# Kernel optimization log

Measured on AMD Instinct MI355X. Metric: run time of the kernel, lower is better.

The kernel has to match this reference:

```python
import jax, jax.numpy as jnp
import numpy as np

B, N, IN_DIM, HEADS, PER_HEAD = 8, 512, 256, 4, 32
OUT_DIM = HEADS * PER_HEAD  # 128
NEG_SLOPE = 0.2


def setup_inputs() -> dict:
    key = jax.random.key(0)
    ks = jax.random.split(key, 8)
    x = jax.random.normal(ks[0], (B, N, IN_DIM), jnp.float32)
    adj = jax.random.randint(ks[1], (B, N, N), 0, 2, jnp.int32)
    sl = 1.0 / np.sqrt(IN_DIM)
    W_l = jax.random.normal(ks[2], (IN_DIM, OUT_DIM), jnp.float32) * sl  # source proj
    b_l = jnp.zeros((OUT_DIM,), jnp.float32)
    W_r = jax.random.normal(ks[3], (IN_DIM, OUT_DIM), jnp.float32) * sl  # target proj
    b_r = jnp.zeros((OUT_DIM,), jnp.float32)
    att = jax.random.normal(ks[4], (HEADS, PER_HEAD), jnp.float32) * (1.0 / np.sqrt(PER_HEAD))
    bias = jnp.zeros((OUT_DIM,), jnp.float32)
    return {"x": x, "adj": adj, "W_l": W_l, "b_l": b_l, "W_r": W_r, "b_r": b_r,
            "att": att, "bias": bias}


def _gatv2_single(x_b, adj_b, W_l, b_l, W_r, b_r, att, bias):
    # PyG GATv2Conv: remove_self_loops + add_self_loops -> diagonal forced to 1
    n = x_b.shape[0]
    adj_sl = jnp.fill_diagonal(adj_b, 1, inplace=False)
    # edge_index = adj.nonzero().t(): source = row, target = col
    m = (adj_sl != 0).T  # m[i, j]: source j feeds target i
    xl = (x_b @ W_l + b_l).reshape(n, HEADS, PER_HEAD)  # source-side features
    xr = (x_b @ W_r + b_r).reshape(n, HEADS, PER_HEAD)  # target-side features
    s = xr[:, None] + xl[None, :]                       # [i, j, H, C]
    s = jnp.where(s > 0, s, NEG_SLOPE * s)              # LeakyReLU(0.2)
    e = jnp.einsum('ijhc,hc->ijh', s, att)              # attention logits
    e = jnp.where(m[..., None], e, -jnp.inf)
    alpha = jax.nn.softmax(e, axis=1)                   # softmax over sources j
    out = jnp.einsum('ijh,jhc->ihc', alpha, xl).reshape(n, HEADS * PER_HEAD)
    return out + bias


def reference(x, adj, W_l, b_l, W_r, b_r, att, bias):
    # Sequential per-batch processing, faithful to the original Python loop
    # and keeping the [N,N,H,C] intermediate to one graph at a time.
    def one(args):
        x_b, adj_b = args
        return _gatv2_single(x_b, adj_b, W_l, b_l, W_r, b_r, att, bias)
    return jax.lax.map(one, (x, adj))  # [B, N, OUT_DIM]
```

## Files before the change

### kernel.cpp

```cpp
#include <hip/hip_runtime.h>
#include <hip/hip_bf16.h>

#define B_   8
#define N_   512
#define IND  256
#define H_   4
#define PH   32
#define OD   128
#define TI   4
#define TJ   64
#define XLS_STRIDE 132

__global__ __launch_bounds__(256, 2) void proj_kernel(
    const float* __restrict__ x,
    const float* __restrict__ Wl, const float* __restrict__ bl,
    const float* __restrict__ Wr, const float* __restrict__ br,
    const float* __restrict__ att,
    float* __restrict__ xl, float* __restrict__ xr,
    float* __restrict__ dl, float* __restrict__ dr)
{
    __shared__ float xs[8 * IND];
    const int t = threadIdx.x;
    const int row0 = blockIdx.x * 8;

    const float4* xp4 = (const float4*)(x + (size_t)row0 * IND);
    float4* xs4 = (float4*)xs;
    #pragma unroll
    for (int k = 0; k < 2; ++k)
        xs4[t + k * 256] = xp4[t + k * 256];
    __syncthreads();

    const int which = t >> 7;
    const int rg = (t >> 6) & 1;
    const int og = t & 63;
    const int o0 = og * 2;
    const int r0 = rg * 4;
    const float* W  = which ? Wr : Wl;
    const float* bb = which ? br : bl;

    float acc0[4], acc1[4];
    #pragma unroll
    for (int r = 0; r < 4; ++r) { acc0[r] = 0.f; acc1[r] = 0.f; }

    for (int k = 0; k < IND; k += 4) {
        float wf0[4], wf1[4];
        #pragma unroll
        for (int kk = 0; kk < 4; ++kk) {
            float2 wv = *(const float2*)(W + (size_t)(k + kk) * OD + o0);
            wf0[kk] = wv.x;
            wf1[kk] = wv.y;
        }
        float xv[4][4];
        #pragma unroll
        for (int r = 0; r < 4; ++r)
            *(float4*)(xv[r]) = *(const float4*)(&xs[(r0 + r) * IND + k]);
        #pragma unroll
        for (int kk = 0; kk < 4; ++kk)
            #pragma unroll
            for (int r = 0; r < 4; ++r) {
                acc0[r] = fmaf(xv[r][kk], wf0[kk], acc0[r]);
                acc1[r] = fmaf(xv[r][kk], wf1[kk], acc1[r]);
            }
    }

    const float bv0 = bb[o0];
    const float bv1 = bb[o0 + 1];
    const float a0 = att[o0];
    const float a1 = att[o0 + 1];
    float* dst = which ? xr : xl;
    float* dp  = which ? dr : dl;
    float dcon[4];
    #pragma unroll
    for (int r = 0; r < 4; ++r) {
        float y0 = acc0[r] + bv0;
        float y1 = acc1[r] + bv1;
        *(float2*)(&dst[(size_t)(row0 + r0 + r) * OD + o0]) = make_float2(y0, y1);
        dcon[r] = fmaf(a0, y0, a1 * y1);
    }
    #pragma unroll
    for (int m = 1; m < 16; m <<= 1) {
        #pragma unroll
        for (int r = 0; r < 4; ++r)
            dcon[r] += __shfl_xor(dcon[r], m);
    }
    if ((og & 15) == 0) {
        const int h = og >> 4;
        #pragma unroll
        for (int r = 0; r < 4; ++r)
            dp[(size_t)(row0 + r0 + r) * H_ + h] = dcon[r];
    }
}

__global__ __launch_bounds__(256, 2) void attn_kernel(
    const int* __restrict__ adj, const float* __restrict__ att,
    const float* __restrict__ bias,
    const float* __restrict__ xl, const float* __restrict__ xr,
    const float* __restrict__ dl, const float* __restrict__ dr,
    float* __restrict__ out)
{
    __shared__ float xls[TJ * XLS_STRIDE];
    __shared__ float masks[TJ * TI];

    const int t = threadIdx.x;
    const int b  = blockIdx.x >> 7;
    const int i0 = (blockIdx.x & 127) * TI;
    const int ch = t & 1;
    const int q  = (t >> 1) & 7;
    const int il = (t >> 4) & 3;
    const int h  = t >> 6;
    const int ig = i0 + il;
    const int cbase = h * PH + ch * 16;

    float attv[16], xrv[16];
    {
        const float* xrp = xr + ((size_t)(b * N_ + ig)) * OD + cbase;
        #pragma unroll
        for (int k = 0; k < 16; k += 4) {
            float4 v = *(const float4*)(xrp + k);
            xrv[k] = v.x; xrv[k+1] = v.y; xrv[k+2] = v.z; xrv[k+3] = v.w;
        }
        const float* ap = att + cbase;
        #pragma unroll
        for (int k = 0; k < 16; ++k) attv[k] = ap[k];
    }
    const float c0 = 0.6f * dr[((size_t)(b * N_ + ig)) * H_ + h];

    float acc[16];
    #pragma unroll
    for (int k = 0; k < 16; ++k) acc[k] = 0.f;
    float sumw = 0.f;

    const float* xlb = xl + (size_t)b * N_ * OD;
    const float* dlb = dl + (size_t)b * N_ * H_;
    const int* adjb  = adj + (size_t)b * N_ * N_;

    for (int tile = 0; tile < N_ / TJ; ++tile) {
        const int j0 = tile * TJ;
        __syncthreads();
        #pragma unroll
        for (int k = 0; k < 8; ++k) {
            int idx = t + k * 256;
            int jj = idx >> 5, m = idx & 31;
            *(float4*)(&xls[jj * XLS_STRIDE + m * 4]) =
                *(const float4*)(xlb + (size_t)(j0 + jj) * OD + m * 4);
        }
        {
            int jj = t >> 2, ii = t & 3;
            int jg2 = j0 + jj, ig2 = i0 + ii;
            int a = adjb[(size_t)jg2 * N_ + ig2];
            masks[t] = (a != 0 || jg2 == ig2) ? 1.f : 0.f;
        }
        __syncthreads();
        float dlv[8];
        #pragma unroll
        for (int u = 0; u < 8; ++u)
            dlv[u] = dlb[(size_t)(j0 + q + u * 8) * H_ + h];
        #pragma unroll 2
        for (int u = 0; u < 8; ++u) {
            const int jj = q + u * 8;
            const float* vrow = &xls[jj * XLS_STRIDE + cbase];
            float v[16];
            #pragma unroll
            for (int k = 0; k < 16; k += 4) {
                float4 w4 = *(const float4*)(vrow + k);
                v[k] = w4.x; v[k+1] = w4.y; v[k+2] = w4.z; v[k+3] = w4.w;
            }
            float ea = 0.f, eb = 0.f, ec = 0.f, ed = 0.f;
            #pragma unroll
            for (int k = 0; k < 16; k += 4) {
                ea = fmaf(attv[k+0], fabsf(xrv[k+0] + v[k+0]), ea);
                eb = fmaf(attv[k+1], fabsf(xrv[k+1] + v[k+1]), eb);
                ec = fmaf(attv[k+2], fabsf(xrv[k+2] + v[k+2]), ec);
                ed = fmaf(attv[k+3], fabsf(xrv[k+3] + v[k+3]), ed);
            }
            float e2h = (ea + eb) + (ec + ed);
            float e2 = e2h + __shfl_xor(e2h, 1);
            float e = fmaf(0.6f, dlv[u], c0);
            e = fmaf(0.4f, e2, e);
            float w = masks[jj * TI + il] * __expf(e);
            sumw += w;
            #pragma unroll
            for (int k = 0; k < 16; ++k) acc[k] = fmaf(w, v[k], acc[k]);
        }
    }

    sumw += __shfl_xor(sumw, 2);
    sumw += __shfl_xor(sumw, 4);
    sumw += __shfl_xor(sumw, 8);
    const float inv = 1.f / sumw;

    float r8[8];
    {
        const bool hi = (q & 4) != 0;
        #pragma unroll
        for (int m = 0; m < 8; ++m) {
            float send = hi ? acc[m] : acc[8 + m];
            float keep = hi ? acc[8 + m] : acc[m];
            r8[m] = keep + __shfl_xor(send, 8);
        }
    }
    float r4[4];
    {
        const bool hi = (q & 2) != 0;
        #pragma unroll
        for (int m = 0; m < 4; ++m) {
            float send = hi ? r8[m] : r8[4 + m];
            float keep = hi ? r8[4 + m] : r8[m];
            r4[m] = keep + __shfl_xor(send, 4);
        }
    }
    float r2[2];
    {
        const bool hi = (q & 1) != 0;
        #pragma unroll
        for (int m = 0; m < 2; ++m) {
            float send = hi ? r4[m] : r4[2 + m];
            float keep = hi ? r4[2 + m] : r4[m];
            r2[m] = keep + __shfl_xor(send, 2);
        }
    }

    const int c = cbase + q * 2;
    float* op = out + ((size_t)(b * N_ + ig)) * OD;
    *(float2*)(&op[c]) = make_float2(fmaf(r2[0], inv, bias[c]),
                                     fmaf(r2[1], inv, bias[c + 1]));
}

extern "C" void kernel_launch(void* const* d_in, const int* in_sizes, int n_in,
                              void* d_out, int out_size, void* d_ws, size_t ws_size,
                              hipStream_t stream) {
    const float* x    = (const float*)d_in[0];
    const int*   adj  = (const int*)d_in[1];
    const float* Wl   = (const float*)d_in[2];
    const float* bl   = (const float*)d_in[3];
    const float* Wr   = (const float*)d_in[4];
    const float* br   = (const float*)d_in[5];
    const float* att  = (const float*)d_in[6];
    const float* bias = (const float*)d_in[7];
    float* out = (float*)d_out;

    float* xl = (float*)d_ws;
    float* xr = xl + (size_t)B_ * N_ * OD;
    float* dl = xr + (size_t)B_ * N_ * OD;
    float* dr = dl + (size_t)B_ * N_ * H_;

    proj_kernel<<<512, 256, 0, stream>>>(x, Wl, bl, Wr, br, att, xl, xr, dl, dr);
    attn_kernel<<<1024, 256, 0, stream>>>(adj, att, bias, xl, xr, dl, dr, out);
}
```

Before: 132.7 us.

## Use async global-to-LDS copies, packed FMA math, DPP reduction, remapped lanes

The xl tile is now loaded with global_load_lds direct-to-LDS copies into an unpadded buffer, which avoids staging the data through registers. The inner score and accumulate loops use 2-wide float vectors so the compiler can emit packed FP32 FMAs, and 0.4 is folded into att. The cross-lane partner sum uses DPP instead of a shuffle. The thread-to-(i,q) mapping is changed, so the final reduction uses different xor distances and a permuted output column. Removing the padding may cause LDS bank conflicts, and the occupancy hint of 2 is dropped.

```diff
diff --git a/kernel.cpp b/kernel.cpp
--- a/kernel.cpp
+++ b/kernel.cpp
@@ -9,7 +9,20 @@
 #define OD   128
 #define TI   4
 #define TJ   64
-#define XLS_STRIDE 132
+
+typedef float v2f __attribute__((ext_vector_type(2)));
+
+__device__ __forceinline__ float dpp_xor1_add(float x) {
+    int yi = __builtin_amdgcn_mov_dpp(__float_as_int(x), 0xB1, 0xF, 0xF, true);
+    return x + __int_as_float(yi);
+}
+
+__device__ __forceinline__ void async_copy16(void* lds_base_uniform, const void* g_perlane) {
+    __builtin_amdgcn_global_load_lds(
+        (const __attribute__((address_space(1))) unsigned*)g_perlane,
+        (__attribute__((address_space(3))) unsigned*)lds_base_uniform,
+        16, 0, 0);
+}
 
 __global__ __launch_bounds__(256, 2) void proj_kernel(
     const float* __restrict__ x,
@@ -91,58 +104,62 @@
     }
 }
 
-__global__ __launch_bounds__(256, 2) void attn_kernel(
+__global__ __launch_bounds__(256) void attn_kernel(
     const int* __restrict__ adj, const float* __restrict__ att,
     const float* __restrict__ bias,
     const float* __restrict__ xl, const float* __restrict__ xr,
     const float* __restrict__ dl, const float* __restrict__ dr,
     float* __restrict__ out)
 {
-    __shared__ float xls[TJ * XLS_STRIDE];
+    __shared__ float xls[TJ * OD];
     __shared__ float masks[TJ * TI];
 
     const int t = threadIdx.x;
     const int b  = blockIdx.x >> 7;
     const int i0 = (blockIdx.x & 127) * TI;
     const int ch = t & 1;
-    const int q  = (t >> 1) & 7;
-    const int il = (t >> 4) & 3;
+    const int il = (t >> 1) & 3;
+    const int q  = (t >> 3) & 7;
     const int h  = t >> 6;
+    const int lane = t & 63;
+    const int wv = __builtin_amdgcn_readfirstlane(t >> 6);
     const int ig = i0 + il;
     const int cbase = h * PH + ch * 16;
 
-    float attv[16], xrv[16];
+    v2f attv[8], xrv[8];
     {
         const float* xrp = xr + ((size_t)(b * N_ + ig)) * OD + cbase;
-        #pragma unroll
-        for (int k = 0; k < 16; k += 4) {
-            float4 v = *(const float4*)(xrp + k);
-            xrv[k] = v.x; xrv[k+1] = v.y; xrv[k+2] = v.z; xrv[k+3] = v.w;
-        }
-        const float* ap = att + cbase;
-        #pragma unroll
-        for (int k = 0; k < 16; ++k) attv[k] = ap[k];
+        const float* ap  = att + cbase;
+        #pragma unroll
+        for (int k = 0; k < 4; ++k) {
+            float4 v = *(const float4*)(xrp + k * 4);
+            xrv[2*k]   = (v2f){v.x, v.y};
+            xrv[2*k+1] = (v2f){v.z, v.w};
+            float4 a = *(const float4*)(ap + k * 4);
+            attv[2*k]   = (v2f){0.4f * a.x, 0.4f * a.y};
+            attv[2*k+1] = (v2f){0.4f * a.z, 0.4f * a.w};
+        }
     }
     const float c0 = 0.6f * dr[((size_t)(b * N_ + ig)) * H_ + h];
 
-    float acc[16];
-    #pragma unroll
-    for (int k = 0; k < 16; ++k) acc[k] = 0.f;
+    v2f acc2[8];
+    #pragma unroll
+    for (int m = 0; m < 8; ++m) acc2[m] = (v2f){0.f, 0.f};
     float sumw = 0.f;
 
     const float* xlb = xl + (size_t)b * N_ * OD;
-    const float* dlb = dl + (size_t)b * N_ * H_;
     const int* adjb  = adj + (size_t)b * N_ * N_;
 
     for (int tile = 0; tile < N_ / TJ; ++tile) {
         const int j0 = tile * TJ;
         __syncthreads();
-        #pragma unroll
-        for (int k = 0; k < 8; ++k) {
-            int idx = t + k * 256;
-            int jj = idx >> 5, m = idx & 31;
-            *(float4*)(&xls[jj * XLS_STRIDE + m * 4]) =
-                *(const float4*)(xlb + (size_t)(j0 + jj) * OD + m * 4);
+        {
+            const float* gsrc = xlb + (size_t)j0 * OD;
+            #pragma unroll
+            for (int k = 0; k < 8; ++k) {
+                const int base4 = k * 256 + wv * 64;
+                async_copy16(&xls[base4 * 4], gsrc + (size_t)(base4 + lane) * 4);
+            }
         }
         {
             int jj = t >> 2, ii = t & 3;
@@ -151,51 +168,61 @@
             masks[t] = (a != 0 || jg2 == ig2) ? 1.f : 0.f;
         }
         __syncthreads();
-        float dlv[8];
+
+        const float* dlt = dl + ((size_t)b * N_ + j0) * H_ + h;
+        float ebase[8];
         #pragma unroll
         for (int u = 0; u < 8; ++u)
-            dlv[u] = dlb[(size_t)(j0 + q + u * 8) * H_ + h];
-        #pragma unroll 2
+            ebase[u] = fmaf(0.6f, dlt[(q + u * 8) * H_], c0);
+
+        #pragma unroll
         for (int u = 0; u < 8; ++u) {
             const int jj = q + u * 8;
-            const float* vrow = &xls[jj * XLS_STRIDE + cbase];
-            float v[16];
-            #pragma unroll
-            for (int k = 0; k < 16; k += 4) {
-                float4 w4 = *(const float4*)(vrow + k);
-                v[k] = w4.x; v[k+1] = w4.y; v[k+2] = w4.z; v[k+3] = w4.w;
+            const float* vrow = &xls[jj * OD + cbase];
+            float4 f0 = *(const float4*)(vrow + 0);
+            float4 f1 = *(const float4*)(vrow + 4);
+            float4 f2 = *(const float4*)(vrow + 8);
+            float4 f3 = *(const float4*)(vrow + 12);
+            v2f vv[8] = {{f0.x,f0.y},{f0.z,f0.w},{f1.x,f1.y},{f1.z,f1.w},
+                         {f2.x,f2.y},{f2.z,f2.w},{f3.x,f3.y},{f3.z,f3.w}};
+            v2f e2a = (v2f){0.f, 0.f}, e2b = (v2f){0.f, 0.f};
+            #pragma unroll
+            for (int m = 0; m < 8; m += 2) {
+                v2f s0 = xrv[m] + vv[m];
+                v2f s1 = xrv[m+1] + vv[m+1];
+                v2f a0 = __builtin_elementwise_max(s0, -s0);
+                v2f a1 = __builtin_elementwise_max(s1, -s1);
+                e2a = __builtin_elementwise_fma(attv[m],   a0, e2a);
+                e2b = __builtin_elementwise_fma(attv[m+1], a1, e2b);
             }
-            float ea = 0.f, eb = 0.f, ec = 0.f, ed = 0.f;
-            #pragma unroll
-            for (int k = 0; k < 16; k += 4) {
-                ea = fmaf(attv[k+0], fabsf(xrv[k+0] + v[k+0]), ea);
-                eb = fmaf(attv[k+1], fabsf(xrv[k+1] + v[k+1]), eb);
-                ec = fmaf(attv[k+2], fabsf(xrv[k+2] + v[k+2]), ec);
-                ed = fmaf(attv[k+3], fabsf(xrv[k+3] + v[k+3]), ed);
-            }
-            float e2h = (ea + eb) + (ec + ed);
-            float e2 = e2h + __shfl_xor(e2h, 1);
-            float e = fmaf(0.6f, dlv[u], c0);
-            e = fmaf(0.4f, e2, e);
+            v2f e2v = e2a + e2b;
+            float e2h = e2v.x + e2v.y;
+            float e = ebase[u] + dpp_xor1_add(e2h);
             float w = masks[jj * TI + il] * __expf(e);
             sumw += w;
-            #pragma unroll
-            for (int k = 0; k < 16; ++k) acc[k] = fmaf(w, v[k], acc[k]);
-        }
-    }
-
-    sumw += __shfl_xor(sumw, 2);
-    sumw += __shfl_xor(sumw, 4);
+            v2f wv2 = (v2f){w, w};
+            #pragma unroll
+            for (int m = 0; m < 8; ++m)
+                acc2[m] = __builtin_elementwise_fma(wv2, vv[m], acc2[m]);
+        }
+    }
+
     sumw += __shfl_xor(sumw, 8);
+    sumw += __shfl_xor(sumw, 16);
+    sumw += __shfl_xor(sumw, 32);
     const float inv = 1.f / sumw;
 
+    float accf[16];
+    #pragma unroll
+    for (int m = 0; m < 8; ++m) { accf[2*m] = acc2[m].x; accf[2*m+1] = acc2[m].y; }
+
     float r8[8];
     {
-        const bool hi = (q & 4) != 0;
+        const bool hi = (q & 1) != 0;
         #pragma unroll
         for (int m = 0; m < 8; ++m) {
-            float send = hi ? acc[m] : acc[8 + m];
-            float keep = hi ? acc[8 + m] : acc[m];
+            float send = hi ? accf[m] : accf[8 + m];
+            float keep = hi ? accf[8 + m] : accf[m];
             r8[m] = keep + __shfl_xor(send, 8);
         }
     }
@@ -206,21 +233,22 @@
         for (int m = 0; m < 4; ++m) {
             float send = hi ? r8[m] : r8[4 + m];
             float keep = hi ? r8[4 + m] : r8[m];
-            r4[m] = keep + __shfl_xor(send, 4);
+            r4[m] = keep + __shfl_xor(send, 16);
         }
     }
     float r2[2];
     {
-        const bool hi = (q & 1) != 0;
+        const bool hi = (q & 4) != 0;
         #pragma unroll
         for (int m = 0; m < 2; ++m) {
             float send = hi ? r4[m] : r4[2 + m];
             float keep = hi ? r4[2 + m] : r4[m];
-            r2[m] = keep + __shfl_xor(send, 2);
-        }
-    }
-
-    const int c = cbase + q * 2;
+            r2[m] = keep + __shfl_xor(send, 32);
+        }
+    }
+
+    const int off = (q & 1) * 8 + ((q >> 1) & 1) * 4 + ((q >> 2) & 1) * 2;
+    const int c = cbase + off;
     float* op = out + ((size_t)(b * N_ + ig)) * OD;
     *(float2*)(&op[c]) = make_float2(fmaf(r2[0], inv, bias[c]),
                                      fmaf(r2[1], inv, bias[c + 1]));
```

Result: slower. 158.0 us (+19.0%).

## Restructure GATv2 attention to register-prefetch sources and reuse across targets

Applied to the files above, without the earlier changes.

Replaces the LDS-tiled attention loop with a scheme where each thread streams source rows straight from global memory with one-step register prefetch and reuses each loaded row across all four target nodes. The LDS staging and its per-tile barriers go away, and a single LDS reduction across 16 source slices finishes the job. The exponent constants are folded into att and dl/dr so the kernel can use a raw exp2, and the code uses packed float2 math plus DPP adds for the head reduction. Occupancy is raised to 3 blocks per CU. The trade-offs are more global/L2 traffic per block for xl, and heavier register pressure from holding four targets' accumulators.

```diff
diff --git a/kernel.cpp b/kernel.cpp
--- a/kernel.cpp
+++ b/kernel.cpp
@@ -8,8 +8,25 @@
 #define PH   32
 #define OD   128
 #define TI   4
-#define TJ   64
-#define XLS_STRIDE 132
+
+typedef float v2f __attribute__((ext_vector_type(2)));
+
+#define ATT_SCALE 0.5770780163555854f
+#define DLR_SCALE 0.8656170245333781f
+
+template <int PAT>
+__device__ __forceinline__ float dpp_add(float x) {
+    int yi = __builtin_amdgcn_mov_dpp(__float_as_int(x), PAT, 0xF, 0xF, true);
+    return x + __int_as_float(yi);
+}
+
+__device__ __forceinline__ float fast_exp2(float x) {
+#if __has_builtin(__builtin_amdgcn_exp2f)
+    return __builtin_amdgcn_exp2f(x);
+#else
+    return exp2f(x);
+#endif
+}
 
 __global__ __launch_bounds__(256, 2) void proj_kernel(
     const float* __restrict__ x,
@@ -87,143 +104,147 @@
         const int h = og >> 4;
         #pragma unroll
         for (int r = 0; r < 4; ++r)
-            dp[(size_t)(row0 + r0 + r) * H_ + h] = dcon[r];
-    }
-}
-
-__global__ __launch_bounds__(256, 2) void attn_kernel(
+            dp[(size_t)(row0 + r0 + r) * H_ + h] = DLR_SCALE * dcon[r];
+    }
+}
+
+__global__ __launch_bounds__(256, 3) void attn_kernel(
     const int* __restrict__ adj, const float* __restrict__ att,
     const float* __restrict__ bias,
     const float* __restrict__ xl, const float* __restrict__ xr,
     const float* __restrict__ dl, const float* __restrict__ dr,
     float* __restrict__ out)
 {
-    __shared__ float xls[TJ * XLS_STRIDE];
-    __shared__ float masks[TJ * TI];
+    __shared__ float sacc[H_][16][TI][PH];
+    __shared__ float ssum[H_][16][TI];
 
     const int t = threadIdx.x;
     const int b  = blockIdx.x >> 7;
     const int i0 = (blockIdx.x & 127) * TI;
-    const int ch = t & 1;
-    const int q  = (t >> 1) & 7;
-    const int il = (t >> 4) & 3;
+    const int cq = t & 3;
+    const int js = (t >> 2) & 15;
     const int h  = t >> 6;
-    const int ig = i0 + il;
-    const int cbase = h * PH + ch * 16;
-
-    float attv[16], xrv[16];
+    const int cbase = h * PH + cq * 8;
+
+    v2f attv[4];
     {
-        const float* xrp = xr + ((size_t)(b * N_ + ig)) * OD + cbase;
-        #pragma unroll
-        for (int k = 0; k < 16; k += 4) {
-            float4 v = *(const float4*)(xrp + k);
-            xrv[k] = v.x; xrv[k+1] = v.y; xrv[k+2] = v.z; xrv[k+3] = v.w;
+        const float* ap = att + cbase;
+        float4 a0 = *(const float4*)(ap);
+        float4 a1 = *(const float4*)(ap + 4);
+        attv[0] = (v2f){ATT_SCALE * a0.x, ATT_SCALE * a0.y};
+        attv[1] = (v2f){ATT_SCALE * a0.z, ATT_SCALE * a0.w};
+        attv[2] = (v2f){ATT_SCALE * a1.x, ATT_SCALE * a1.y};
+        attv[3] = (v2f){ATT_SCALE * a1.z, ATT_SCALE * a1.w};
+    }
+    v2f xrv[TI][4];
+    float drv[TI];
+    #pragma unroll
+    for (int il = 0; il < TI; ++il) {
+        const float* xp = xr + ((size_t)(b * N_ + i0 + il)) * OD + cbase;
+        float4 r0 = *(const float4*)(xp);
+        float4 r1 = *(const float4*)(xp + 4);
+        xrv[il][0] = (v2f){r0.x, r0.y};
+        xrv[il][1] = (v2f){r0.z, r0.w};
+        xrv[il][2] = (v2f){r1.x, r1.y};
+        xrv[il][3] = (v2f){r1.z, r1.w};
+        drv[il] = dr[((size_t)(b * N_ + i0 + il)) * H_ + h];
+    }
+
+    v2f acc[TI][4];
+    float sumw[TI];
+    #pragma unroll
+    for (int il = 0; il < TI; ++il) {
+        sumw[il] = 0.f;
+        #pragma unroll
+        for (int m = 0; m < 4; ++m) acc[il][m] = (v2f){0.f, 0.f};
+    }
+
+    const float* xlp = xl + ((size_t)(b * N_ + js)) * OD + cbase;
+    const int*   ajp = adj + ((size_t)(b * N_ + js)) * N_ + i0;
+    const float* dlp = dl + ((size_t)(b * N_ + js)) * H_ + h;
+
+    float4 va = *(const float4*)(xlp);
+    float4 vb = *(const float4*)(xlp + 4);
+    int4   mj = *(const int4*)(ajp);
+    float  dj = *dlp;
+
+    #pragma unroll 2
+    for (int u = 0; u < 32; ++u) {
+        float4 wa = va, wb = vb;
+        int4   wm = mj;
+        float  wd = dj;
+        if (u < 31) {
+            xlp += 16 * OD; ajp += 16 * N_; dlp += 16 * H_;
+            va = *(const float4*)(xlp);
+            vb = *(const float4*)(xlp + 4);
+            mj = *(const int4*)(ajp);
+            dj = *dlp;
         }
-        const float* ap = att + cbase;
-        #pragma unroll
-        for (int k = 0; k < 16; ++k) attv[k] = ap[k];
-    }
-    const float c0 = 0.6f * dr[((size_t)(b * N_ + ig)) * H_ + h];
-
-    float acc[16];
-    #pragma unroll
-    for (int k = 0; k < 16; ++k) acc[k] = 0.f;
-    float sumw = 0.f;
-
-    const float* xlb = xl + (size_t)b * N_ * OD;
-    const float* dlb = dl + (size_t)b * N_ * H_;
-    const int* adjb  = adj + (size_t)b * N_ * N_;
-
-    for (int tile = 0; tile < N_ / TJ; ++tile) {
-        const int j0 = tile * TJ;
-        __syncthreads();
-        #pragma unroll
-        for (int k = 0; k < 8; ++k) {
-            int idx = t + k * 256;
-            int jj = idx >> 5, m = idx & 31;
-            *(float4*)(&xls[jj * XLS_STRIDE + m * 4]) =
-                *(const float4*)(xlb + (size_t)(j0 + jj) * OD + m * 4);
+        const int j = u * 16 + js;
+        v2f v0 = (v2f){wa.x, wa.y}, v1 = (v2f){wa.z, wa.w};
+        v2f v2 = (v2f){wb.x, wb.y}, v3 = (v2f){wb.z, wb.w};
+        int wmv[4] = {wm.x, wm.y, wm.z, wm.w};
+        #pragma unroll
+        for (int il = 0; il < TI; ++il) {
+            v2f s, e0 = (v2f){0.f, 0.f}, e1 = (v2f){0.f, 0.f};
+            s = xrv[il][0] + v0; s = __builtin_elementwise_max(s, -s);
+            e0 = __builtin_elementwise_fma(attv[0], s, e0);
+            s = xrv[il][1] + v1; s = __builtin_elementwise_max(s, -s);
+            e1 = __builtin_elementwise_fma(attv[1], s, e1);
+            s = xrv[il][2] + v2; s = __builtin_elementwise_max(s, -s);
+            e0 = __builtin_elementwise_fma(attv[2], s, e0);
+            s = xrv[il][3] + v3; s = __builtin_elementwise_max(s, -s);
+            e1 = __builtin_elementwise_fma(attv[3], s, e1);
+            v2f et = e0 + e1;
+            float eh = et.x + et.y;
+            eh = dpp_add<0xB1>(eh);
+            eh = dpp_add<0x4E>(eh);
+            float e = (wd + drv[il]) + eh;
+            bool keep = (wmv[il] != 0) || (j == i0 + il);
+            float w = keep ? fast_exp2(e) : 0.f;
+            sumw[il] += w;
+            v2f wv2 = (v2f){w, w};
+            acc[il][0] = __builtin_elementwise_fma(wv2, v0, acc[il][0]);
+            acc[il][1] = __builtin_elementwise_fma(wv2, v1, acc[il][1]);
+            acc[il][2] = __builtin_elementwise_fma(wv2, v2, acc[il][2]);
+            acc[il][3] = __builtin_elementwise_fma(wv2, v3, acc[il][3]);
         }
-        {
-            int jj = t >> 2, ii = t & 3;
-            int jg2 = j0 + jj, ig2 = i0 + ii;
-            int a = adjb[(size_t)jg2 * N_ + ig2];
-            masks[t] = (a != 0 || jg2 == ig2) ? 1.f : 0.f;
-        }
-        __syncthreads();
-        float dlv[8];
-        #pragma unroll
-        for (int u = 0; u < 8; ++u)
-            dlv[u] = dlb[(size_t)(j0 + q + u * 8) * H_ + h];
-        #pragma unroll 2
-        for (int u = 0; u < 8; ++u) {
-            const int jj = q + u * 8;
-            const float* vrow = &xls[jj * XLS_STRIDE + cbase];
-            float v[16];
-            #pragma unroll
-            for (int k = 0; k < 16; k += 4) {
-                float4 w4 = *(const float4*)(vrow + k);
-                v[k] = w4.x; v[k+1] = w4.y; v[k+2] = w4.z; v[k+3] = w4.w;
-            }
-            float ea = 0.f, eb = 0.f, ec = 0.f, ed = 0.f;
-            #pragma unroll
-            for (int k = 0; k < 16; k += 4) {
-                ea = fmaf(attv[k+0], fabsf(xrv[k+0] + v[k+0]), ea);
-                eb = fmaf(attv[k+1], fabsf(xrv[k+1] + v[k+1]), eb);
-                ec = fmaf(attv[k+2], fabsf(xrv[k+2] + v[k+2]), ec);
-                ed = fmaf(attv[k+3], fabsf(xrv[k+3] + v[k+3]), ed);
-            }
-            float e2h = (ea + eb) + (ec + ed);
-            float e2 = e2h + __shfl_xor(e2h, 1);
-            float e = fmaf(0.6f, dlv[u], c0);
-            e = fmaf(0.4f, e2, e);
-            float w = masks[jj * TI + il] * __expf(e);
-            sumw += w;
-            #pragma unroll
-            for (int k = 0; k < 16; ++k) acc[k] = fmaf(w, v[k], acc[k]);
-        }
-    }
-
-    sumw += __shfl_xor(sumw, 2);
-    sumw += __shfl_xor(sumw, 4);
-    sumw += __shfl_xor(sumw, 8);
-    const float inv = 1.f / sumw;
-
-    float r8[8];
-    {
-        const bool hi = (q & 4) != 0;
-        #pragma unroll
-        for (int m = 0; m < 8; ++m) {
-            float send = hi ? acc[m] : acc[8 + m];
-            float keep = hi ? acc[8 + m] : acc[m];
-            r8[m] = keep + __shfl_xor(send, 8);
-        }
-    }
-    float r4[4];
-    {
-        const bool hi = (q & 2) != 0;
-        #pragma unroll
-        for (int m = 0; m < 4; ++m) {
-            float send = hi ? r8[m] : r8[4 + m];
-            float keep = hi ? r8[4 + m] : r8[m];
-            r4[m] = keep + __shfl_xor(send, 4);
-        }
-    }
-    float r2[2];
-    {
-        const bool hi = (q & 1) != 0;
-        #pragma unroll
-        for (int m = 0; m < 2; ++m) {
-            float send = hi ? r4[m] : r4[2 + m];
-            float keep = hi ? r4[2 + m] : r4[m];
-            r2[m] = keep + __shfl_xor(send, 2);
-        }
-    }
-
-    const int c = cbase + q * 2;
-    float* op = out + ((size_t)(b * N_ + ig)) * OD;
-    *(float2*)(&op[c]) = make_float2(fmaf(r2[0], inv, bias[c]),
-                                     fmaf(r2[1], inv, bias[c + 1]));
+    }
+
+    #pragma unroll
+    for (int il = 0; il < TI; ++il) {
+        float4 w0 = make_float4(acc[il][0].x, acc[il][0].y,
+                                acc[il][1].x, acc[il][1].y);
+        float4 w1 = make_float4(acc[il][2].x, acc[il][2].y,
+                                acc[il][3].x, acc[il][3].y);
+        *(float4*)(&sacc[h][js][il][cq * 8])     = w0;
+        *(float4*)(&sacc[h][js][il][cq * 8 + 4]) = w1;
+    }
+    if (cq == 0) {
+        #pragma unroll
+        for (int il = 0; il < TI; ++il)
+            ssum[h][js][il] = sumw[il];
+    }
+    __syncthreads();
+
+    const int lane = t & 63;
+    const int o = lane * 2;
+    const int il2 = o >> 5;
+    const int c2 = o & 31;
+    float st = 0.f;
+    #pragma unroll
+    for (int k = 0; k < 16; ++k) st += ssum[h][k][il2];
+    float a0 = 0.f, a1 = 0.f;
+    #pragma unroll
+    for (int k = 0; k < 16; ++k) {
+        float2 p = *(const float2*)(&sacc[h][k][il2][c2]);
+        a0 += p.x; a1 += p.y;
+    }
+    const float inv = 1.f / st;
+    const int c = h * PH + c2;
+    float* op = out + ((size_t)(b * N_ + i0 + il2)) * OD;
+    *(float2*)(&op[c]) = make_float2(fmaf(a0, inv, bias[c]),
+                                     fmaf(a1, inv, bias[c + 1]));
 }
 
 extern "C" void kernel_launch(void* const* d_in, const int* in_sizes, int n_in,
```

New measurement: 125.2 us. 1.06x faster.
